# Optimization experiments

Hardware: AMD Instinct MI355X
Metric: run time of the kernel (lower is better)

The kernel has to match this reference:

```python
import jax, jax.numpy as jnp
import numpy as np

D_MODEL = 1024
D_STATE = 16
D_CONV = 4
EXPAND = 2
D_INNER = EXPAND * D_MODEL
DT_RANK = -(-D_MODEL // 16)  # ceil(d_model/16) = 64
LN_EPS = 1e-5


def setup_inputs() -> dict:
    key = jax.random.key(0)
    ks = jax.random.split(key, 10)
    b, l = 1, 2048
    s = 0.02
    x = jax.random.normal(ks[0], (b, l, D_MODEL), dtype=jnp.float32)
    gamma = jnp.ones((D_MODEL,), jnp.float32)
    beta = jnp.zeros((D_MODEL,), jnp.float32)
    w_in = jax.random.normal(ks[1], (2 * D_INNER, D_MODEL), jnp.float32) * s
    conv_w = jax.random.normal(ks[2], (D_INNER, D_CONV), jnp.float32) * s
    conv_b = jnp.zeros((D_INNER,), jnp.float32)
    w_x = jax.random.normal(ks[3], (DT_RANK + 2 * D_STATE, D_INNER), jnp.float32) * s
    w_dt = jax.random.normal(ks[4], (D_INNER, DT_RANK), jnp.float32) * s
    b_dt = jax.random.normal(ks[5], (D_INNER,), jnp.float32) * s
    A_log = jnp.log(jnp.broadcast_to(jnp.arange(1, D_STATE + 1, dtype=jnp.float32)[None, :], (D_INNER, D_STATE)))
    Dp = jnp.ones((D_INNER,), jnp.float32)
    w_out = jax.random.normal(ks[6], (D_MODEL, D_INNER), jnp.float32) * s
    return {"x": x, "gamma": gamma, "beta": beta, "w_in": w_in, "conv_w": conv_w,
            "conv_b": conv_b, "w_x": w_x, "w_dt": w_dt, "b_dt": b_dt,
            "A_log": A_log, "Dp": Dp, "w_out": w_out}


def _combine(e1, e2):
    # (a2, b2) o (a1, b1) = (a2*a1, a2*b1 + b2); e2 is the later element
    a1, b1 = e1
    a2, b2 = e2
    return (a2 * a1, a2 * b1 + b2)


def _forward(x, gamma, beta, w_in, conv_w, conv_b, w_x, w_dt, b_dt, A_log, Dp, w_out):
    residual = x
    # LayerNorm
    mu = jnp.mean(x, axis=-1, keepdims=True)
    var = jnp.var(x, axis=-1, keepdims=True)
    xn = (x - mu) * jax.lax.rsqrt(var + LN_EPS) * gamma + beta
    # in_proj and split
    xz = jnp.einsum('bld,ed->ble', xn, w_in)
    x_part, z = xz[..., :D_INNER], xz[..., D_INNER:]
    # causal depthwise conv1d (torch pads k-1 both sides then trims to l == left pad)
    lhs = jnp.transpose(x_part, (0, 2, 1))  # (b, d_inner, l)
    rhs = conv_w[:, None, :]                # (d_inner, 1, k)
    conv = jax.lax.conv_general_dilated(
        lhs, rhs, window_strides=(1,), padding=[(D_CONV - 1, 0)],
        dimension_numbers=('NCH', 'OIH', 'NCH'), feature_group_count=D_INNER)
    x_part = jnp.transpose(conv, (0, 2, 1)) + conv_b  # (b, l, d_inner)
    x_part = jax.nn.silu(x_part)  # dropout is identity in eval mode
    # SSM
    A = -jnp.exp(A_log)  # (d_inner, n)
    x_dbl = jnp.einsum('bld,ed->ble', x_part, w_x)
    dt = x_dbl[..., :DT_RANK]
    B = x_dbl[..., DT_RANK:DT_RANK + D_STATE]
    C = x_dbl[..., DT_RANK + D_STATE:]
    delta = jax.nn.softplus(jnp.einsum('blr,dr->bld', dt, w_dt) + b_dt)  # (b,l,d_inner)
    deltaA = jnp.exp(delta[..., None] * A[None, None])                    # (b,l,d_inner,n)
    dBu = delta[..., None] * B[:, :, None, :] * x_part[..., None]         # (b,l,d_inner,n)
    _, h = jax.lax.associative_scan(_combine, (deltaA, dBu), axis=1)
    y = jnp.sum(h * C[:, :, None, :], axis=-1) + x_part * Dp             # (b,l,d_inner)
    y = y * jax.nn.silu(z)
    out = jnp.einsum('ble,de->bld', y, w_out) + residual
    return out


def reference(x, gamma, beta, w_in, conv_w, conv_b, w_x, w_dt, b_dt, A_log, Dp, w_out):
    return _forward(x, gamma, beta, w_in, conv_w, conv_b, w_x, w_dt, b_dt, A_log, Dp, w_out)
```

## Files before the change

### kernel.cpp

```cpp
#include <hip/hip_runtime.h>
#include <math.h>

#define L_SEQ 2048
#define DM 1024
#define DI 2048
#define DS 16
#define DR 64
#define XDN 96
#define NCHUNK 64
#define TCH 32
#define KSLICES 8
#define KSL (DI / KSLICES)

typedef __attribute__((ext_vector_type(8))) short bf16x8;
typedef __attribute__((ext_vector_type(4))) float f32x4;
typedef unsigned short ushort_t;
typedef __attribute__((address_space(1))) const unsigned int GU32;
typedef __attribute__((address_space(3))) unsigned int LU32;

__device__ inline unsigned short f2bf(float f) {
  unsigned int u = __builtin_bit_cast(unsigned int, f);
  u += 0x7fffu + ((u >> 16) & 1u);
  return (unsigned short)(u >> 16);
}
__device__ inline float bf2f(unsigned short u) {
  return __builtin_bit_cast(float, (unsigned int)u << 16);
}

__device__ inline void cvt4(const float* src, ushort_t* dst, int j) {
  float4 v = ((const float4*)src)[j];
  ushort4 o;
  o.x = f2bf(v.x); o.y = f2bf(v.y); o.z = f2bf(v.z); o.w = f2bf(v.w);
  ((ushort4*)dst)[j] = o;
}

__global__ void cvt_all_kernel(const float* __restrict__ w_in,
                               const float* __restrict__ w_out,
                               const float* __restrict__ w_x,
                               const float* __restrict__ w_dt,
                               ushort_t* __restrict__ w_inb,
                               ushort_t* __restrict__ w_outb,
                               ushort_t* __restrict__ w_xb,
                               ushort_t* __restrict__ w_dtb) {
  int i = blockIdx.x * 256 + threadIdx.x;
  const int N0 = 2 * DI * DM / 4;
  const int N1 = N0 + DM * DI / 4;
  const int N2 = N1 + 128 * DI / 4;
  const int N3 = N2 + DI * DR / 4;
  if (i < N0) {
    cvt4(w_in, w_inb, i);
  } else if (i < N1) {
    cvt4(w_out, w_outb, i - N0);
  } else if (i < N2) {
    int j = i - N1;
    int e0 = j << 2;
    int row = e0 >> 11;
    int col = e0 & (DI - 1);
    ushort4 o = {0, 0, 0, 0};
    if (row < XDN) {
      float4 v = *(const float4*)(w_x + (size_t)row * DI + col);
      o.x = f2bf(v.x); o.y = f2bf(v.y); o.z = f2bf(v.z); o.w = f2bf(v.w);
    }
    ((ushort4*)w_xb)[j] = o;
  } else if (i < N3) {
    cvt4(w_dt, w_dtb, i - N2);
  }
}

__global__ void ln_kernel(const float* __restrict__ x,
                          const float* __restrict__ gamma,
                          const float* __restrict__ beta,
                          ushort_t* __restrict__ xnb) {
  int row = blockIdx.x;
  int t = threadIdx.x;
  const float4* xr = (const float4*)(x + (size_t)row * DM);
  float4 v = xr[t];
  float s = v.x + v.y + v.z + v.w;
  float s2 = v.x * v.x + v.y * v.y + v.z * v.z + v.w * v.w;
#pragma unroll
  for (int off = 32; off > 0; off >>= 1) {
    s += __shfl_down(s, off);
    s2 += __shfl_down(s2, off);
  }
  __shared__ float ls[4], ls2[4];
  if ((t & 63) == 0) { ls[t >> 6] = s; ls2[t >> 6] = s2; }
  __syncthreads();
  float tot = ls[0] + ls[1] + ls[2] + ls[3];
  float tot2 = ls2[0] + ls2[1] + ls2[2] + ls2[3];
  float mu = tot * (1.0f / DM);
  float var = tot2 * (1.0f / DM) - mu * mu;
  float r = rsqrtf(var + 1e-5f);
  float4 g = ((const float4*)gamma)[t];
  float4 b = ((const float4*)beta)[t];
  ushort4 o;
  o.x = f2bf((v.x - mu) * r * g.x + b.x);
  o.y = f2bf((v.y - mu) * r * g.y + b.y);
  o.z = f2bf((v.z - mu) * r * g.z + b.z);
  o.w = f2bf((v.w - mu) * r * g.w + b.w);
  ((ushort4*)(xnb + (size_t)row * DM))[t] = o;
}

template <int EPI>
__global__ __launch_bounds__(256) void mgemm(
    const ushort_t* __restrict__ A, int lda,
    const ushort_t* __restrict__ B, int ldb,
    void* __restrict__ Cp, int ldc, int ksl,
    const float* __restrict__ extra) {
  __shared__ ushort_t As[128 * 64];
  __shared__ ushort_t Bs[128 * 64];
  const int tid = threadIdx.x;
  const int lane = tid & 63;
  const int wave = tid >> 6;
  const int m0 = blockIdx.y * 128;
  const int n0 = blockIdx.x * 128;
  const int kbase = blockIdx.z * ksl;
  const int wr = (wave >> 1) * 64;
  const int wc = (wave & 1) * 64;
  const int kq = lane >> 4;
  const int rr = lane & 15;
  f32x4 acc[4][4];
#pragma unroll
  for (int i = 0; i < 4; ++i)
#pragma unroll
    for (int j = 0; j < 4; ++j) acc[i][j] = (f32x4){0.f, 0.f, 0.f, 0.f};

  int ur[4], uc[4];
#pragma unroll
  for (int q = 0; q < 4; ++q) {
    int u = tid + 256 * q;
    ur[q] = u >> 3;
    uc[q] = (((u & 7) ^ (ur[q] & 7)) << 3);
  }

  for (int k0 = kbase; k0 < kbase + ksl; k0 += 64) {
    __syncthreads();
#pragma unroll
    for (int q = 0; q < 4; ++q)
      __builtin_amdgcn_global_load_lds(
          (GU32*)(A + (size_t)(m0 + ur[q]) * lda + k0 + uc[q]),
          (LU32*)(As + (tid + 256 * q) * 8), 16, 0, 0);
#pragma unroll
    for (int q = 0; q < 4; ++q)
      __builtin_amdgcn_global_load_lds(
          (GU32*)(B + (size_t)(n0 + ur[q]) * ldb + k0 + uc[q]),
          (LU32*)(Bs + (tid + 256 * q) * 8), 16, 0, 0);
    __syncthreads();
#pragma unroll
    for (int kk = 0; kk < 2; ++kk) {
      const int sw = ((rr & 7) << 4);
      bf16x8 a[4], b[4];
#pragma unroll
      for (int i = 0; i < 4; ++i) {
        int row = wr + i * 16 + rr;
        int off = ((kk * 64 + kq * 16) ^ sw);
        a[i] = *(const bf16x8*)((const char*)As + row * 128 + off);
      }
#pragma unroll
      for (int j = 0; j < 4; ++j) {
        int row = wc + j * 16 + rr;
        int off = ((kk * 64 + kq * 16) ^ sw);
        b[j] = *(const bf16x8*)((const char*)Bs + row * 128 + off);
      }
#pragma unroll
      for (int i = 0; i < 4; ++i)
#pragma unroll
        for (int j = 0; j < 4; ++j)
          acc[i][j] = __builtin_amdgcn_mfma_f32_16x16x32_bf16(a[i], b[j], acc[i][j], 0, 0, 0);
    }
  }
#pragma unroll
  for (int i = 0; i < 4; ++i) {
#pragma unroll
    for (int j = 0; j < 4; ++j) {
#pragma unroll
      for (int r = 0; r < 4; ++r) {
        int row = m0 + wr + i * 16 + kq * 4 + r;
        int col = n0 + wc + j * 16 + rr;
        float v = acc[i][j][r];
        if (EPI == 4) {
          ((ushort_t*)Cp)[(size_t)row * ldc + col] = f2bf(v);
        } else if (EPI == 5) {
          v += extra[col];
          v = (v > 20.f) ? v : __logf(1.f + __expf(v));
          ((ushort_t*)Cp)[(size_t)row * ldc + col] = f2bf(v);
        } else if (EPI == 6) {
          ((float*)Cp)[((size_t)blockIdx.z * L_SEQ + row) * ldc + col] = v;
        }
      }
    }
  }
}

__global__ void reduce_xdbl_kernel(const float* __restrict__ part,
                                   float* __restrict__ xdbl,
                                   ushort_t* __restrict__ dtb) {
  int i = blockIdx.x * 256 + threadIdx.x;
  int col = i & 127;
  int row = i >> 7;
  float s = 0.f;
#pragma unroll
  for (int k = 0; k < KSLICES; ++k) s += part[(size_t)k * (L_SEQ * 128) + i];
  if (col < DR) dtb[(size_t)row * DR + col] = f2bf(s);
  if (col < XDN) xdbl[(size_t)row * XDN + col] = s;
}

__global__ void reduce_out_kernel(const float* __restrict__ part,
                                  const float* __restrict__ x,
                                  float* __restrict__ out) {
  int i = blockIdx.x * 256 + threadIdx.x;
  float4 p0 = ((const float4*)part)[i];
  float4 p1 = ((const float4*)(part + (size_t)L_SEQ * DM))[i];
  float4 xr = ((const float4*)x)[i];
  float4 o;
  o.x = p0.x + p1.x + xr.x;
  o.y = p0.y + p1.y + xr.y;
  o.z = p0.z + p1.z + xr.z;
  o.w = p0.w + p1.w + xr.w;
  ((float4*)out)[i] = o;
}

__global__ void conv_silu_kernel(const ushort_t* __restrict__ xzb,
                                 const float* __restrict__ conv_w,
                                 const float* __restrict__ conv_b,
                                 ushort_t* __restrict__ xconvb) {
  int i = blockIdx.x * blockDim.x + threadIdx.x;
  int d0 = (i & (DI / 4 - 1)) << 2;
  int t = i >> 9;
  float4 bia = *(const float4*)(conv_b + d0);
  float acc[4] = {bia.x, bia.y, bia.z, bia.w};
  float w[4][4];
#pragma unroll
  for (int c = 0; c < 4; ++c) {
    float4 wv = *(const float4*)(conv_w + (size_t)(d0 + c) * 4);
    w[c][0] = wv.x; w[c][1] = wv.y; w[c][2] = wv.z; w[c][3] = wv.w;
  }
#pragma unroll
  for (int j = 0; j < 4; ++j) {
    int tt = t - 3 + j;
    if (tt >= 0) {
      ushort4 xv = *(const ushort4*)(xzb + (size_t)tt * (2 * DI) + d0);
      acc[0] += bf2f(xv.x) * w[0][j];
      acc[1] += bf2f(xv.y) * w[1][j];
      acc[2] += bf2f(xv.z) * w[2][j];
      acc[3] += bf2f(xv.w) * w[3][j];
    }
  }
  ushort4 o;
  o.x = f2bf(acc[0] / (1.f + __expf(-acc[0])));
  o.y = f2bf(acc[1] / (1.f + __expf(-acc[1])));
  o.z = f2bf(acc[2] / (1.f + __expf(-acc[2])));
  o.w = f2bf(acc[3] / (1.f + __expf(-acc[3])));
  *(ushort4*)(xconvb + (size_t)t * DI + d0) = o;
}

__global__ void scan_chunk_kernel(const ushort_t* __restrict__ deltab,
                                  const ushort_t* __restrict__ ub,
                                  const float* __restrict__ xdbl,
                                  const float* __restrict__ A_log,
                                  float* __restrict__ P,
                                  float* __restrict__ HB) {
  int d = blockIdx.x * blockDim.x + threadIdx.x;
  int c = blockIdx.y;
  int t0 = c * TCH;
  float Aval[DS];
#pragma unroll
  for (int q = 0; q < 4; ++q) {
    float4 al = *(const float4*)(A_log + (size_t)d * DS + q * 4);
    Aval[q * 4 + 0] = -__expf(al.x);
    Aval[q * 4 + 1] = -__expf(al.y);
    Aval[q * 4 + 2] = -__expf(al.z);
    Aval[q * 4 + 3] = -__expf(al.w);
  }
  float h[DS], p[DS];
#pragma unroll
  for (int n = 0; n < DS; ++n) { h[n] = 0.f; p[n] = 1.f; }
  for (int t = t0; t < t0 + TCH; ++t) {
    float dlt = bf2f(deltab[(size_t)t * DI + d]);
    float uv = bf2f(ub[(size_t)t * DI + d]);
    float du = dlt * uv;
    float Bv[DS];
#pragma unroll
    for (int q = 0; q < 4; ++q) {
      float4 b4 = *(const float4*)(xdbl + (size_t)t * XDN + DR + q * 4);
      Bv[q * 4 + 0] = b4.x; Bv[q * 4 + 1] = b4.y;
      Bv[q * 4 + 2] = b4.z; Bv[q * 4 + 3] = b4.w;
    }
#pragma unroll
    for (int n = 0; n < DS; ++n) {
      float dA = __expf(dlt * Aval[n]);
      p[n] *= dA;
      h[n] = dA * h[n] + du * Bv[n];
    }
  }
#pragma unroll
  for (int n = 0; n < DS; ++n) {
    size_t idx = ((size_t)c * DS + n) * DI + d;
    P[idx] = p[n];
    HB[idx] = h[n];
  }
}

__global__ void scan_prop_kernel(const float* __restrict__ P,
                                 const float* __restrict__ HB,
                                 float* __restrict__ HIN) {
  int dn = blockIdx.x * blockDim.x + threadIdx.x;
  float h = 0.f;
#pragma unroll 4
  for (int c = 0; c < NCHUNK; ++c) {
    size_t idx = (size_t)c * (DI * DS) + dn;
    HIN[idx] = h;
    h = P[idx] * h + HB[idx];
  }
}

__global__ void scan_final_kernel(const ushort_t* __restrict__ deltab,
                                  const ushort_t* __restrict__ ub,
                                  const float* __restrict__ xdbl,
                                  const ushort_t* __restrict__ xzb,
                                  const float* __restrict__ A_log,
                                  const float* __restrict__ Dp,
                                  const float* __restrict__ HIN,
                                  ushort_t* __restrict__ ygb) {
  int d = blockIdx.x * blockDim.x + threadIdx.x;
  int c = blockIdx.y;
  int t0 = c * TCH;
  float Aval[DS];
#pragma unroll
  for (int q = 0; q < 4; ++q) {
    float4 al = *(const float4*)(A_log + (size_t)d * DS + q * 4);
    Aval[q * 4 + 0] = -__expf(al.x);
    Aval[q * 4 + 1] = -__expf(al.y);
    Aval[q * 4 + 2] = -__expf(al.z);
    Aval[q * 4 + 3] = -__expf(al.w);
  }
  float Dval = Dp[d];
  float h[DS];
#pragma unroll
  for (int n = 0; n < DS; ++n) h[n] = HIN[((size_t)c * DS + n) * DI + d];
  for (int t = t0; t < t0 + TCH; ++t) {
    float dlt = bf2f(deltab[(size_t)t * DI + d]);
    float uv = bf2f(ub[(size_t)t * DI + d]);
    float du = dlt * uv;
    float Bv[DS], Cv[DS];
#pragma unroll
    for (int q = 0; q < 4; ++q) {
      float4 b4 = *(const float4*)(xdbl + (size_t)t * XDN + DR + q * 4);
      float4 c4 = *(const float4*)(xdbl + (size_t)t * XDN + DR + DS + q * 4);
      Bv[q * 4 + 0] = b4.x; Bv[q * 4 + 1] = b4.y;
      Bv[q * 4 + 2] = b4.z; Bv[q * 4 + 3] = b4.w;
      Cv[q * 4 + 0] = c4.x; Cv[q * 4 + 1] = c4.y;
      Cv[q * 4 + 2] = c4.z; Cv[q * 4 + 3] = c4.w;
    }
    float acc = uv * Dval;
#pragma unroll
    for (int n = 0; n < DS; ++n) {
      float dA = __expf(dlt * Aval[n]);
      h[n] = dA * h[n] + du * Bv[n];
      acc += h[n] * Cv[n];
    }
    float z = bf2f(xzb[(size_t)t * (2 * DI) + DI + d]);
    float sz = z / (1.f + __expf(-z));
    ygb[(size_t)t * DI + d] = f2bf(acc * sz);
  }
}

extern "C" void kernel_launch(void* const* d_in, const int* in_sizes, int n_in,
                              void* d_out, int out_size, void* d_ws, size_t ws_size,
                              hipStream_t stream) {
  const float* x = (const float*)d_in[0];
  const float* gamma = (const float*)d_in[1];
  const float* beta = (const float*)d_in[2];
  const float* w_in = (const float*)d_in[3];
  const float* conv_w = (const float*)d_in[4];
  const float* conv_b = (const float*)d_in[5];
  const float* w_x = (const float*)d_in[6];
  const float* w_dt = (const float*)d_in[7];
  const float* b_dt = (const float*)d_in[8];
  const float* A_log = (const float*)d_in[9];
  const float* Dp = (const float*)d_in[10];
  const float* w_out = (const float*)d_in[11];
  float* out = (float*)d_out;

  float* ws = (float*)d_ws;
  float* xdbl = ws;
  float* P = xdbl + (size_t)L_SEQ * XDN;
  float* HB = P + (size_t)NCHUNK * DI * DS;
  float* HIN = HB + (size_t)NCHUNK * DI * DS;
  float* part = HIN + (size_t)NCHUNK * DI * DS;
  ushort_t* xzb = (ushort_t*)(part + (size_t)KSLICES * L_SEQ * 128);
  ushort_t* xconvb = xzb + (size_t)L_SEQ * 2 * DI;
  ushort_t* deltab = xconvb + (size_t)L_SEQ * DI;
  ushort_t* ygb = deltab + (size_t)L_SEQ * DI;
  ushort_t* xnb = ygb + (size_t)L_SEQ * DI;
  ushort_t* w_inb = xnb + (size_t)L_SEQ * DM;
  ushort_t* w_outb = w_inb + (size_t)(2 * DI) * DM;
  ushort_t* w_xb = w_outb + (size_t)DM * DI;
  ushort_t* w_dtb = w_xb + (size_t)128 * DI;
  ushort_t* dtb = w_dtb + (size_t)DI * DR;
  float* part_out = (float*)xzb;

  {
    int units = (2 * DI * DM + DM * DI + 128 * DI + DI * DR) / 4;
    cvt_all_kernel<<<(units + 255) / 256, 256, 0, stream>>>(
        w_in, w_out, w_x, w_dt, w_inb, w_outb, w_xb, w_dtb);
  }
  ln_kernel<<<L_SEQ, 256, 0, stream>>>(x, gamma, beta, xnb);
  mgemm<4><<<dim3((2 * DI) / 128, L_SEQ / 128, 1), 256, 0, stream>>>(
      xnb, DM, w_inb, DM, xzb, 2 * DI, DM, nullptr);
  conv_silu_kernel<<<(L_SEQ * DI / 4) / 256, 256, 0, stream>>>(
      xzb, conv_w, conv_b, xconvb);
  mgemm<6><<<dim3(1, L_SEQ / 128, KSLICES), 256, 0, stream>>>(
      xconvb, DI, w_xb, DI, part, 128, KSL, nullptr);
  reduce_xdbl_kernel<<<(L_SEQ * 128) / 256, 256, 0, stream>>>(part, xdbl, dtb);
  mgemm<5><<<dim3(DI / 128, L_SEQ / 128, 1), 256, 0, stream>>>(
      dtb, DR, w_dtb, DR, deltab, DI, DR, b_dt);
  scan_chunk_kernel<<<dim3(DI / 256, NCHUNK), 256, 0, stream>>>(
      deltab, xconvb, xdbl, A_log, P, HB);
  scan_prop_kernel<<<(DI * DS) / 256, 256, 0, stream>>>(P, HB, HIN);
  scan_final_kernel<<<dim3(DI / 256, NCHUNK), 256, 0, stream>>>(
      deltab, xconvb, xdbl, xzb, A_log, Dp, HIN, ygb);
  mgemm<6><<<dim3(DM / 128, L_SEQ / 128, 2), 256, 0, stream>>>(
      ygb, DI, w_outb, DI, part_out, DM, DI / 2, nullptr);
  reduce_out_kernel<<<(L_SEQ * DM / 4) / 256, 256, 0, stream>>>(part_out, x, out);
}
```

Before: 161.3 us.

## Add triple-buffered async-LDS GEMM for in_proj with 256x128 tiles

Replaces the generic in_proj GEMM with a new kernel that uses 512 threads, 256x128 output tiles, and a three-stage LDS ring filled by global_load_lds direct copies with an XOR swizzle. Staging of tile k+2 is interleaved with MFMA quadrants of tile k, and s_setprio raises wave priority around the MFMA bursts. The aim is to hide global load latency and raise MFMA utilisation in the largest GEMM. In exchange it needs 144KB of dynamic shared memory and hand-tuned vmcnt waits and barriers, which can stall if the counts are wrong.

```diff
diff --git a/kernel.cpp b/kernel.cpp
--- a/kernel.cpp
+++ b/kernel.cpp
@@ -100,6 +100,153 @@
   ((ushort4*)(xnb + (size_t)row * DM))[t] = o;
 }
 
+__device__ __forceinline__ void stage_a_pipe(const ushort_t* A, int lda, int m0,
+                                             int k0, ushort_t* dst, int r, int tid) {
+  int lrow = tid >> 3, slot = tid & 7;
+  int grow = r * 64 + lrow;
+  int scol = ((slot ^ (grow & 7)) << 3);
+  __builtin_amdgcn_global_load_lds(
+      (GU32*)(A + (size_t)(m0 + grow) * lda + k0 + scol),
+      (LU32*)(dst + r * 4096 + tid * 8), 16, 0, 0);
+}
+__device__ __forceinline__ void stage_b_pipe(const ushort_t* B, int ldb, int n0,
+                                             int k0, ushort_t* dst, int r, int tid) {
+  int lrow = tid >> 3, slot = tid & 7;
+  int grow = r * 64 + lrow;
+  int scol = ((slot ^ (grow & 7)) << 3);
+  __builtin_amdgcn_global_load_lds(
+      (GU32*)(B + (size_t)(n0 + grow) * ldb + k0 + scol),
+      (LU32*)(dst + 16384 + r * 4096 + tid * 8), 16, 0, 0);
+}
+
+#define DS_FRAGS(QM, QN)                                                     \
+  bf16x8 af[2][2], bg[2][2];                                                 \
+  {                                                                          \
+    const char* cA = (const char*)pa0;                                       \
+    const char* cB = (const char*)pa0 + 32768;                               \
+    _Pragma("unroll") for (int i = 0; i < 2; ++i) {                          \
+      int fr = wm * 64 + (QM) * 32 + i * 16 + rr;                            \
+      int rb = fr * 128, sw = (fr & 7) << 4;                                 \
+      _Pragma("unroll") for (int kk = 0; kk < 2; ++kk)                       \
+        af[i][kk] = *(const bf16x8*)(cA + rb + ((((kk)*4 + kq) << 4) ^ sw)); \
+    }                                                                        \
+    _Pragma("unroll") for (int j = 0; j < 2; ++j) {                          \
+      int fn = wn * 64 + (QN) * 32 + j * 16 + rr;                            \
+      int rb = fn * 128, sw = (fn & 7) << 4;                                 \
+      _Pragma("unroll") for (int kk = 0; kk < 2; ++kk)                       \
+        bg[j][kk] = *(const bf16x8*)(cB + rb + ((((kk)*4 + kq) << 4) ^ sw)); \
+    }                                                                        \
+  }
+
+#define MFMA_Q(QM, QN)                                                       \
+  __builtin_amdgcn_s_setprio(1);                                             \
+  _Pragma("unroll") for (int i = 0; i < 2; ++i)                              \
+  _Pragma("unroll") for (int j = 0; j < 2; ++j)                              \
+  _Pragma("unroll") for (int kk = 0; kk < 2; ++kk)                           \
+    acc[(QM)*2 + i][(QN)*2 + j] = __builtin_amdgcn_mfma_f32_16x16x32_bf16(   \
+        af[i][kk], bg[j][kk], acc[(QM)*2 + i][(QN)*2 + j], 0, 0, 0);         \
+  __builtin_amdgcn_s_setprio(0);
+
+#define BARRIER_PIN()                                                        \
+  __builtin_amdgcn_s_barrier();                                              \
+  __builtin_amdgcn_sched_barrier(0);
+
+__global__ __launch_bounds__(512, 2) void mgemm_pipe(
+    const ushort_t* __restrict__ A, int lda,
+    const ushort_t* __restrict__ B, int ldb,
+    ushort_t* __restrict__ C, int ldc, int K) {
+  extern __shared__ ushort_t smp[];
+  const int tid = threadIdx.x;
+  const int lane = tid & 63;
+  const int wave = tid >> 6;
+  const int wm = wave >> 1;
+  const int wn = wave & 1;
+  const int kq = lane >> 4;
+  const int rr = lane & 15;
+  const int m0 = blockIdx.y * 256;
+  const int n0 = blockIdx.x * 128;
+  const int NK = K >> 6;
+
+  ushort_t* pa0 = smp;
+  ushort_t* pa1 = smp + 24576;
+  ushort_t* pa2 = smp + 49152;
+
+  f32x4 acc[4][4];
+#pragma unroll
+  for (int i = 0; i < 4; ++i)
+#pragma unroll
+    for (int j = 0; j < 4; ++j) acc[i][j] = (f32x4){0.f, 0.f, 0.f, 0.f};
+
+#pragma unroll
+  for (int r = 0; r < 4; ++r) stage_a_pipe(A, lda, m0, 0, pa0, r, tid);
+#pragma unroll
+  for (int r = 0; r < 2; ++r) stage_b_pipe(B, ldb, n0, 0, pa0, r, tid);
+#pragma unroll
+  for (int r = 0; r < 4; ++r) stage_a_pipe(A, lda, m0, 64, pa1, r, tid);
+#pragma unroll
+  for (int r = 0; r < 2; ++r) stage_b_pipe(B, ldb, n0, 64, pa1, r, tid);
+  asm volatile("s_waitcnt vmcnt(6)" ::: "memory");
+  BARRIER_PIN();
+
+  for (int k = 0; k < NK; ++k) {
+    const bool do_stage = (k < NK - 2);
+    const int k2 = (k + 2) << 6;
+    {
+      DS_FRAGS(0, 0);
+      if (do_stage) {
+        stage_a_pipe(A, lda, m0, k2, pa2, 0, tid);
+        stage_b_pipe(B, ldb, n0, k2, pa2, 0, tid);
+      }
+      BARRIER_PIN();
+      MFMA_Q(0, 0);
+      BARRIER_PIN();
+    }
+    {
+      DS_FRAGS(0, 1);
+      if (do_stage) {
+        stage_a_pipe(A, lda, m0, k2, pa2, 1, tid);
+        stage_b_pipe(B, ldb, n0, k2, pa2, 1, tid);
+      }
+      BARRIER_PIN();
+      MFMA_Q(0, 1);
+      BARRIER_PIN();
+    }
+    {
+      DS_FRAGS(1, 0);
+      if (do_stage) stage_a_pipe(A, lda, m0, k2, pa2, 2, tid);
+      BARRIER_PIN();
+      MFMA_Q(1, 0);
+      BARRIER_PIN();
+    }
+    {
+      DS_FRAGS(1, 1);
+      if (do_stage) stage_a_pipe(A, lda, m0, k2, pa2, 3, tid);
+      if (k < NK - 2) {
+        asm volatile("s_waitcnt vmcnt(6)" ::: "memory");
+      } else if (k == NK - 2) {
+        asm volatile("s_waitcnt vmcnt(0)" ::: "memory");
+      }
+      BARRIER_PIN();
+      MFMA_Q(1, 1);
+      BARRIER_PIN();
+    }
+    ushort_t* t = pa0; pa0 = pa1; pa1 = pa2; pa2 = t;
+  }
+
+#pragma unroll
+  for (int ri = 0; ri < 4; ++ri) {
+#pragma unroll
+    for (int cj = 0; cj < 4; ++cj) {
+#pragma unroll
+      for (int g = 0; g < 4; ++g) {
+        int row = m0 + wm * 64 + ri * 16 + kq * 4 + g;
+        int col = n0 + wn * 64 + cj * 16 + rr;
+        C[(size_t)row * ldc + col] = f2bf(acc[ri][cj][g]);
+      }
+    }
+  }
+}
+
 template <int EPI>
 __global__ __launch_bounds__(256) void mgemm(
     const ushort_t* __restrict__ A, int lda,
@@ -177,9 +324,7 @@
         int row = m0 + wr + i * 16 + kq * 4 + r;
         int col = n0 + wc + j * 16 + rr;
         float v = acc[i][j][r];
-        if (EPI == 4) {
-          ((ushort_t*)Cp)[(size_t)row * ldc + col] = f2bf(v);
-        } else if (EPI == 5) {
+        if (EPI == 5) {
           v += extra[col];
           v = (v > 20.f) ? v : __logf(1.f + __expf(v));
           ((ushort_t*)Cp)[(size_t)row * ldc + col] = f2bf(v);
@@ -405,8 +550,8 @@
         w_in, w_out, w_x, w_dt, w_inb, w_outb, w_xb, w_dtb);
   }
   ln_kernel<<<L_SEQ, 256, 0, stream>>>(x, gamma, beta, xnb);
-  mgemm<4><<<dim3((2 * DI) / 128, L_SEQ / 128, 1), 256, 0, stream>>>(
-      xnb, DM, w_inb, DM, xzb, 2 * DI, DM, nullptr);
+  mgemm_pipe<<<dim3((2 * DI) / 128, L_SEQ / 256), 512, 3 * 24576 * 2, stream>>>(
+      xnb, DM, w_inb, DM, xzb, 2 * DI, DM);
   conv_silu_kernel<<<(L_SEQ * DI / 4) / 256, 256, 0, stream>>>(
       xzb, conv_w, conv_b, xconvb);
   mgemm<6><<<dim3(1, L_SEQ / 128, KSLICES), 256, 0, stream>>>(
```

Result: no change. 163.6 us (+1.4%).
